# Kernel optimization log

Hardware: AMD Instinct MI355X
Metric: run time of the kernel (lower is better)

Reference implementation:

```python
import jax, jax.numpy as jnp
import numpy as np

N_NODES = 50000
N_REL = 500
D_IN = 128
D_OUT = 128
D_REL = 128
NHEADS = 2
ALPHA = 0.2
E1 = 200000   # direct edges
E2 = 50000    # 2-hop paths


def _xavier(key, shape, gain=1.414):
    fan_out, fan_in = shape[-2], shape[-1]
    a = gain * np.sqrt(6.0 / (fan_in + fan_out))
    return jax.random.uniform(key, shape, jnp.float32, -a, a)


def setup_inputs() -> dict:
    key = jax.random.key(0)
    ks = jax.random.split(key, 11)
    return {
        "entity_embeddings": jax.random.normal(ks[0], (N_NODES, D_IN), jnp.float32),
        "relation_embeddings": jax.random.normal(ks[1], (N_REL, D_REL), jnp.float32),
        "entity_list": jax.random.randint(ks[2], (2, E1), 0, N_NODES),
        "relation_type": jax.random.randint(ks[3], (E1,), 0, N_REL),
        "entity_list_nhop": jax.random.randint(ks[4], (2, E2), 0, N_NODES),
        "relation_type_nhop": jax.random.randint(ks[5], (E2, 2), 0, N_REL),
        # per-head attention params: a [out, 2*in + nrela], a2 [out] (squeezed [1,out])
        "a_heads": _xavier(ks[6], (NHEADS, D_OUT, 2 * D_IN + D_REL)),
        "a2_heads": _xavier(ks[7], (NHEADS, 1, D_OUT))[:, 0, :],
        "W": _xavier(ks[8], (D_REL, NHEADS * D_OUT)),
        "a_out": _xavier(ks[9], (NHEADS * D_OUT, 3 * NHEADS * D_OUT)),
        "a2_out": _xavier(ks[10], (1, NHEADS * D_OUT))[0],
    }


def _sp_att(x, edge, eemb, a, a2, concat):
    """SpGraphAttentionLayer. x:[N,Din] edge:[2,E] eemb:[E,Drel] a:[Dout,2Din+Drel] a2:[Dout]."""
    din = x.shape[1]
    src = x[edge[0]]                       # [E, Din]
    dst = x[edge[1]]                       # [E, Din]
    # a.mm(edge_h) without materializing the [E, 2Din+Drel] concat
    edge_m = (src @ a[:, :din].T
              + dst @ a[:, din:2 * din].T
              + eemb @ a[:, 2 * din:].T)   # [E, Dout]
    edge_e = jnp.exp(-jax.nn.leaky_relu(edge_m @ a2, ALPHA))      # [E]
    rowsum = jax.ops.segment_sum(edge_e, edge[0], num_segments=x.shape[0])  # [N]
    rowsum = jnp.where(rowsum == 0.0, 1e-12, rowsum)
    h = jax.ops.segment_sum(edge_e[:, None] * edge_m, edge[0], num_segments=x.shape[0])
    h = h / rowsum[:, None]                # [N, Dout]
    return jax.nn.elu(h) if concat else h


def reference(entity_embeddings, relation_embeddings, entity_list, relation_type,
              entity_list_nhop, relation_type_nhop, a_heads, a2_heads, W, a_out, a2_out):
    ent, rel = entity_embeddings, relation_embeddings
    edge_all = jnp.concatenate([entity_list, entity_list_nhop], axis=1)   # [2, E1+E2]

    # layer-1 edge embeddings
    emb_nhop = (rel[relation_type_nhop[:, 0]] + rel[relation_type_nhop[:, 1]]
                + ent[entity_list_nhop[0]] + ent[entity_list_nhop[1]])
    edge_embed = rel[relation_type] + ent[entity_list[0]] + ent[entity_list[1]]
    eemb1 = jnp.concatenate([edge_embed, emb_nhop], axis=0)               # [E1+E2, Drel]

    # multi-head sparse attention, concat heads (torch.cat dim=1 == (N,H,D)->reshape)
    heads = jax.vmap(lambda a, a2: _sp_att(ent, edge_all, eemb1, a, a2, True))(a_heads, a2_heads)
    out1 = jnp.transpose(heads, (1, 0, 2)).reshape(ent.shape[0], -1)      # [N, H*Dout]
    # dropout p=0.0 -> identity

    out_rel = rel @ W                                                      # [R, H*Dout]
    edge_embed2 = out_rel[relation_type]
    emb_nhop2 = (out_rel[relation_type_nhop[:, 0]] + out_rel[relation_type_nhop[:, 1]]
                 + out1[entity_list_nhop[0]] + out1[entity_list_nhop[1]])
    eemb2 = jnp.concatenate([edge_embed2, emb_nhop2], axis=0)

    out_ent = jax.nn.elu(_sp_att(out1, edge_all, eemb2, a_out, a2_out, False))
    return out_ent, out_rel
```

## Files before the change

kernel.cpp:

```cpp
#include <hip/hip_runtime.h>
#include <math.h>

#define NN   50000
#define NR   500
#define E1N  200000
#define E2N  50000
#define EN   250000
#define ALPHAC 0.2f

#define OFF_OUT1  ((size_t)0)
#define OFF_EE1   ((size_t)51200000)
#define OFF_EE2   ((size_t)53200000)
#define OFF_W1    ((size_t)54200000)
#define OFF_W2    ((size_t)54203072)
#define OFF_DEG   ((size_t)54206144)
#define OFF_OFFS  ((size_t)54406144)
#define OFF_CUR   ((size_t)54606208)
#define OFF_BSUM  ((size_t)54806208)
#define OFF_CARRY ((size_t)54807232)
#define OFF_CSR   ((size_t)54808256)
#define OFF_AHH   ((size_t)55808256)
#define OFF_AHL   ((size_t)56004864)
#define OFF_AOH   ((size_t)56201472)
#define OFF_AOL   ((size_t)56594688)

typedef __attribute__((ext_vector_type(8))) short bf16x8;
typedef __attribute__((ext_vector_type(4))) short short4v;
typedef __attribute__((ext_vector_type(2))) short short2v;
typedef __attribute__((ext_vector_type(4))) float f4;
typedef __attribute__((ext_vector_type(2))) float f2;
typedef __attribute__((ext_vector_type(4))) float f32x4;

__device__ __forceinline__ float lrelu(float x) { return x > 0.f ? x : ALPHAC * x; }
__device__ __forceinline__ float eluf(float x)  { return x > 0.f ? x : expm1f(x); }

__device__ __forceinline__ short bfh(float x) {
    union { float f; unsigned u; } c; c.f = x;
    unsigned r = (c.u + 0x7FFFu + ((c.u >> 16) & 1u)) >> 16;
    return (short)r;
}
__device__ __forceinline__ float bf2f(short h) {
    union { unsigned u; float f; } c; c.u = ((unsigned)(unsigned short)h) << 16;
    return c.f;
}

__device__ __forceinline__ void decode_edge(int e, const int* el1, const int* rt1,
                                            const int* el2, const int* rtn,
                                            int& src, int& dst, int& ra, int& rb) {
    if (e < E1N) {
        src = el1[e]; dst = el1[E1N + e]; ra = rt1[e]; rb = -1;
    } else {
        int j = e - E1N;
        src = el2[j]; dst = el2[E2N + j]; ra = rtn[2 * j]; rb = rtn[2 * j + 1];
    }
}

__global__ void k_w(const float* aH, const float* a2H, const float* aO, const float* a2O,
                    float* w1, float* w2) {
    int t = blockIdx.x * blockDim.x + threadIdx.x;
    if (t < 768) {
        int h = t / 384; int r = t - h * 384; int seg = r >> 7; int j = r & 127;
        const float* A  = aH + (size_t)h * 128 * 384;
        const float* a2 = a2H + h * 128;
        float s = 0.f;
        for (int d = 0; d < 128; ++d) {
            const float* row = A + d * 384;
            float c;
            if (seg == 0)      c = row[j]       + row[256 + j];
            else if (seg == 1) c = row[128 + j] + row[256 + j];
            else               c = row[256 + j];
            s += a2[d] * c;
        }
        w1[t] = s;
    } else if (t < 1536) {
        int r = t - 768; int seg = r >> 8; int j = r & 255;
        float s = 0.f;
        for (int d = 0; d < 256; ++d) s += a2O[d] * aO[d * 768 + seg * 256 + j];
        w2[r] = s;
    }
}

__global__ void k_conv(const float* aH, const float* aO,
                       short* ahh, short* ahl, short* aoh, short* aol) {
    int t = blockIdx.x * 256 + threadIdx.x;
    if (t < 98304) {
        float x = aH[t];
        short hi = bfh(x);
        ahh[t] = hi; ahl[t] = bfh(x - bf2f(hi));
    } else if (t < 294912) {
        int i = t - 98304;
        float x = aO[i];
        short hi = bfh(x);
        aoh[i] = hi; aol[i] = bfh(x - bf2f(hi));
    }
}

__global__ void k_outrel(const float* rel, const float* W, float* outrel) {
    int r = blockIdx.x; int c = threadIdx.x;
    const float* rr = rel + r * 128;
    float s = 0.f;
    for (int k = 0; k < 128; ++k) s += rr[k] * W[k * 256 + c];
    outrel[r * 256 + c] = s;
}

__global__ void k_deg(const int* el1, const int* el2, int* deg) {
    int e = blockIdx.x * 256 + threadIdx.x;
    if (e >= EN) return;
    int src = (e < E1N) ? el1[e] : el2[e - E1N];
    atomicAdd(&deg[src], 1);
}

__global__ void k_scan1(const int* deg, int* offs, int* bsum) {
    __shared__ int s[256];
    int t = threadIdx.x; int i = blockIdx.x * 256 + t;
    int v = (i < NN) ? deg[i] : 0;
    s[t] = v; __syncthreads();
    for (int off = 1; off < 256; off <<= 1) {
        int x = (t >= off) ? s[t - off] : 0;
        __syncthreads(); s[t] += x; __syncthreads();
    }
    if (i < NN) offs[i] = s[t] - v;
    if (t == 255) bsum[blockIdx.x] = s[255];
}

__global__ void k_scan2(int* bsum, int* carry) {
    __shared__ int s[256];
    int t = threadIdx.x;
    int v = (t < 196) ? bsum[t] : 0;
    s[t] = v; __syncthreads();
    for (int off = 1; off < 256; off <<= 1) {
        int x = (t >= off) ? s[t - off] : 0;
        __syncthreads(); s[t] += x; __syncthreads();
    }
    if (t < 196) carry[t] = s[t] - v;
}

__global__ void k_scan3(int* offs, const int* carry) {
    int i = blockIdx.x * 256 + threadIdx.x;
    if (i < NN) offs[i] += carry[blockIdx.x];
}

__global__ void k_scatter(const int* el1, const int* el2, const int* offs,
                          int* cursor, int* csr) {
    int e = blockIdx.x * 256 + threadIdx.x;
    if (e >= EN) return;
    int src = (e < E1N) ? el1[e] : el2[e - E1N];
    int pos = offs[src] + atomicAdd(&cursor[src], 1);
    csr[pos] = e;
}

__global__ void k_ee1(const float* ent, const float* rel,
                      const int* el1, const int* rt1, const int* el2, const int* rtn,
                      const float* w1, float* ee) {
    int wid  = (blockIdx.x * blockDim.x + threadIdx.x) >> 6;
    int lane = threadIdx.x & 63;
    int e0 = wid * 8;
    if (e0 >= EN) return;
    f2 wA0 = *(const f2*)&w1[2 * lane];
    f2 wB0 = *(const f2*)&w1[128 + 2 * lane];
    f2 wC0 = *(const f2*)&w1[256 + 2 * lane];
    f2 wA1 = *(const f2*)&w1[384 + 2 * lane];
    f2 wB1 = *(const f2*)&w1[512 + 2 * lane];
    f2 wC1 = *(const f2*)&w1[640 + 2 * lane];
    int eend = min(e0 + 8, EN);
    for (int e = e0; e < eend; ++e) {
        int src, dst, ra, rb;
        decode_edge(e, el1, rt1, el2, rtn, src, dst, ra, rb);
        f2 es = *(const f2*)&ent[src * 128 + 2 * lane];
        f2 ed = *(const f2*)&ent[dst * 128 + 2 * lane];
        f2 rp = *(const f2*)&rel[ra * 128 + 2 * lane];
        if (rb >= 0) rp += *(const f2*)&rel[rb * 128 + 2 * lane];
        float t0 = es[0] * wA0[0] + es[1] * wA0[1] + ed[0] * wB0[0] + ed[1] * wB0[1]
                 + rp[0] * wC0[0] + rp[1] * wC0[1];
        float t1 = es[0] * wA1[0] + es[1] * wA1[1] + ed[0] * wB1[0] + ed[1] * wB1[1]
                 + rp[0] * wC1[0] + rp[1] * wC1[1];
        #pragma unroll
        for (int off = 32; off; off >>= 1) {
            t0 += __shfl_xor(t0, off, 64);
            t1 += __shfl_xor(t1, off, 64);
        }
        if (lane == 0) {
            ee[e]      = expf(-lrelu(t0));
            ee[EN + e] = expf(-lrelu(t1));
        }
    }
}

#define PK1 392
__global__ __launch_bounds__(512) void k_agg1(
        const float* ent, const float* rel,
        const int* el1, const int* rt1, const int* el2, const int* rtn,
        const int* offs, const int* csr, const float* ee,
        const short* ahh, const short* ahl, float* out1) {
    __shared__ __align__(16) short Yh[16 * 2 * PK1];
    __shared__ __align__(16) short Yl[16 * 2 * PK1];
    __shared__ float RS[16][2];
    int w = threadIdx.x >> 6;
    int lane = threadIdx.x & 63;
    for (int s = 0; s < 2; ++s) {
        int m = w * 2 + s;
        int n = blockIdx.x * 16 + m;
        int start = offs[n];
        int end = (n == NN - 1) ? EN : offs[n + 1];
        f2 en = *(const f2*)&ent[n * 128 + 2 * lane];
        f2 s2a = {0, 0}, sea = {0, 0}, s2b = {0, 0}, seb = {0, 0};
        float rs0 = 0.f, rs1 = 0.f;
        for (int idx = start; idx < end; ++idx) {
            int e = csr[idx];
            int src, dst, ra, rb;
            decode_edge(e, el1, rt1, el2, rtn, src, dst, ra, rb);
            float e0v = ee[e], e1v = ee[EN + e];
            f2 gg = *(const f2*)&ent[dst * 128 + 2 * lane];
            f2 rp = *(const f2*)&rel[ra * 128 + 2 * lane];
            if (rb >= 0) rp += *(const f2*)&rel[rb * 128 + 2 * lane];
            f2 em = rp + en + gg;
            s2a += e0v * gg; sea += e0v * em;
            s2b += e1v * gg; seb += e1v * em;
            rs0 += e0v; rs1 += e1v;
        }
        f2 regs[2][3] = {{rs0 * en, s2a, sea}, {rs1 * en, s2b, seb}};
        #pragma unroll
        for (int hh = 0; hh < 2; ++hh) {
            #pragma unroll
            for (int rg = 0; rg < 3; ++rg) {
                int base = m * 2 * PK1 + hh * PK1 + rg * 128 + 2 * lane;
                short2v vh, vl;
                #pragma unroll
                for (int j = 0; j < 2; ++j) {
                    float v = regs[hh][rg][j];
                    vh[j] = bfh(v);
                    vl[j] = bfh(v - bf2f(vh[j]));
                }
                *(short2v*)&Yh[base] = vh;
                *(short2v*)&Yl[base] = vl;
            }
        }
        if (lane == 0) { RS[m][0] = rs0; RS[m][1] = rs1; }
    }
    __syncthreads();

    int r = lane & 15, g = lane >> 4;
    int h = w >> 2;
    const short* YhB = &Yh[r * 2 * PK1 + h * PK1];
    const short* YlB = &Yl[r * 2 * PK1 + h * PK1];
    int ct0 = 2 * w, ct1 = 2 * w + 1;
    const short* B0h = ahh + (size_t)(ct0 * 16 + r) * 384;
    const short* B0l = ahl + (size_t)(ct0 * 16 + r) * 384;
    const short* B1h = ahh + (size_t)(ct1 * 16 + r) * 384;
    const short* B1l = ahl + (size_t)(ct1 * 16 + r) * 384;
    f32x4 z = {0.f, 0.f, 0.f, 0.f};
    f32x4 hh0 = z, hl0 = z, lh0 = z, hh1 = z, hl1 = z, lh1 = z;
    for (int kt = 0; kt < 12; ++kt) {
        int ko = kt * 32 + g * 8;
        bf16x8 yh = *(const bf16x8*)(YhB + ko);
        bf16x8 yl = *(const bf16x8*)(YlB + ko);
        bf16x8 b0h = *(const bf16x8*)(B0h + ko);
        bf16x8 b0l = *(const bf16x8*)(B0l + ko);
        bf16x8 b1h = *(const bf16x8*)(B1h + ko);
        bf16x8 b1l = *(const bf16x8*)(B1l + ko);
        hh0 = __builtin_amdgcn_mfma_f32_16x16x32_bf16(yh, b0h, hh0, 0, 0, 0);
        hh1 = __builtin_amdgcn_mfma_f32_16x16x32_bf16(yh, b1h, hh1, 0, 0, 0);
        hl0 = __builtin_amdgcn_mfma_f32_16x16x32_bf16(yl, b0h, hl0, 0, 0, 0);
        hl1 = __builtin_amdgcn_mfma_f32_16x16x32_bf16(yl, b1h, hl1, 0, 0, 0);
        lh0 = __builtin_amdgcn_mfma_f32_16x16x32_bf16(yh, b0l, lh0, 0, 0, 0);
        lh1 = __builtin_amdgcn_mfma_f32_16x16x32_bf16(yh, b1l, lh1, 0, 0, 0);
    }
    f32x4 acc0 = hh0 + hl0 + lh0;
    f32x4 acc1 = hh1 + hl1 + lh1;
    #pragma unroll
    for (int q = 0; q < 4; ++q) {
        int m = g * 4 + q;
        float rs = RS[m][h];
        float denom = (rs == 0.f) ? 1e-12f : rs;
        size_t row = (size_t)(blockIdx.x * 16 + m) * 256;
        out1[row + ct0 * 16 + r] = eluf(acc0[q] / denom);
        out1[row + ct1 * 16 + r] = eluf(acc1[q] / denom);
    }
}

__global__ void k_ee2(const float* out1, const float* orel,
                      const int* el1, const int* rt1, const int* el2, const int* rtn,
                      const float* w2, float* ee2) {
    int wid  = (blockIdx.x * blockDim.x + threadIdx.x) >> 6;
    int lane = threadIdx.x & 63;
    int e0 = wid * 8;
    if (e0 >= EN) return;
    f4 wS = *(const f4*)&w2[4 * lane];
    f4 wD = *(const f4*)&w2[256 + 4 * lane];
    f4 wE = *(const f4*)&w2[512 + 4 * lane];
    int eend = min(e0 + 8, EN);
    for (int e = e0; e < eend; ++e) {
        int src, dst, ra, rb;
        decode_edge(e, el1, rt1, el2, rtn, src, dst, ra, rb);
        f4 xs = *(const f4*)&out1[(size_t)src * 256 + 4 * lane];
        f4 xd = *(const f4*)&out1[(size_t)dst * 256 + 4 * lane];
        f4 em = *(const f4*)&orel[ra * 256 + 4 * lane];
        if (rb >= 0) em += *(const f4*)&orel[rb * 256 + 4 * lane] + xs + xd;
        f4 tv = xs * wS + xd * wD + em * wE;
        float t = tv[0] + tv[1] + tv[2] + tv[3];
        #pragma unroll
        for (int off = 32; off; off >>= 1) t += __shfl_xor(t, off, 64);
        if (lane == 0) ee2[e] = expf(-lrelu(t));
    }
}

#define PK2 776
__global__ __launch_bounds__(512) void k_agg2(
        const float* out1, const float* orel,
        const int* el1, const int* rt1, const int* el2, const int* rtn,
        const int* offs, const int* csr, const float* ee2,
        const short* aoh, const short* aol, float* out_ent) {
    __shared__ __align__(16) short Yh[16 * PK2];
    __shared__ __align__(16) short Yl[16 * PK2];
    __shared__ float RS[16];
    int w = threadIdx.x >> 6;
    int lane = threadIdx.x & 63;
    for (int s = 0; s < 2; ++s) {
        int m = w * 2 + s;
        int n = blockIdx.x * 16 + m;
        int start = offs[n];
        int end = (n == NN - 1) ? EN : offs[n + 1];
        f4 on = *(const f4*)&out1[(size_t)n * 256 + 4 * lane];
        f4 s2 = {0, 0, 0, 0}, se = {0, 0, 0, 0};
        float rs = 0.f;
        for (int idx = start; idx < end; ++idx) {
            int e = csr[idx];
            int src, dst, ra, rb;
            decode_edge(e, el1, rt1, el2, rtn, src, dst, ra, rb);
            float ev = ee2[e];
            f4 gg = *(const f4*)&out1[(size_t)dst * 256 + 4 * lane];
            f4 em = *(const f4*)&orel[ra * 256 + 4 * lane];
            if (rb >= 0) em += *(const f4*)&orel[rb * 256 + 4 * lane] + on + gg;
            s2 += ev * gg;
            se += ev * em;
            rs += ev;
        }
        f4 regs[3] = {rs * on, s2, se};
        #pragma unroll
        for (int rg = 0; rg < 3; ++rg) {
            int base = m * PK2 + rg * 256 + 4 * lane;
            short4v vh, vl;
            #pragma unroll
            for (int j = 0; j < 4; ++j) {
                float v = regs[rg][j];
                vh[j] = bfh(v);
                vl[j] = bfh(v - bf2f(vh[j]));
            }
            *(short4v*)&Yh[base] = vh;
            *(short4v*)&Yl[base] = vl;
        }
        if (lane == 0) RS[m] = rs;
    }
    __syncthreads();

    int r = lane & 15, g = lane >> 4;
    const short* YhB = &Yh[r * PK2];
    const short* YlB = &Yl[r * PK2];
    int ct0 = 2 * w, ct1 = 2 * w + 1;
    const short* B0h = aoh + (size_t)(ct0 * 16 + r) * 768;
    const short* B0l = aol + (size_t)(ct0 * 16 + r) * 768;
    const short* B1h = aoh + (size_t)(ct1 * 16 + r) * 768;
    const short* B1l = aol + (size_t)(ct1 * 16 + r) * 768;
    f32x4 z = {0.f, 0.f, 0.f, 0.f};
    f32x4 hh0 = z, hl0 = z, lh0 = z, hh1 = z, hl1 = z, lh1 = z;
    for (int kt = 0; kt < 24; ++kt) {
        int ko = kt * 32 + g * 8;
        bf16x8 yh = *(const bf16x8*)(YhB + ko);
        bf16x8 yl = *(const bf16x8*)(YlB + ko);
        bf16x8 b0h = *(const bf16x8*)(B0h + ko);
        bf16x8 b0l = *(const bf16x8*)(B0l + ko);
        bf16x8 b1h = *(const bf16x8*)(B1h + ko);
        bf16x8 b1l = *(const bf16x8*)(B1l + ko);
        hh0 = __builtin_amdgcn_mfma_f32_16x16x32_bf16(yh, b0h, hh0, 0, 0, 0);
        hh1 = __builtin_amdgcn_mfma_f32_16x16x32_bf16(yh, b1h, hh1, 0, 0, 0);
        hl0 = __builtin_amdgcn_mfma_f32_16x16x32_bf16(yl, b0h, hl0, 0, 0, 0);
        hl1 = __builtin_amdgcn_mfma_f32_16x16x32_bf16(yl, b1h, hl1, 0, 0, 0);
        lh0 = __builtin_amdgcn_mfma_f32_16x16x32_bf16(yh, b0l, lh0, 0, 0, 0);
        lh1 = __builtin_amdgcn_mfma_f32_16x16x32_bf16(yh, b1l, lh1, 0, 0, 0);
    }
    f32x4 acc0 = hh0 + hl0 + lh0;
    f32x4 acc1 = hh1 + hl1 + lh1;
    #pragma unroll
    for (int q = 0; q < 4; ++q) {
        int m = g * 4 + q;
        float rs = RS[m];
        float denom = (rs == 0.f) ? 1e-12f : rs;
        size_t row = (size_t)(blockIdx.x * 16 + m) * 256;
        out_ent[row + ct0 * 16 + r] = eluf(acc0[q] / denom);
        out_ent[row + ct1 * 16 + r] = eluf(acc1[q] / denom);
    }
}

extern "C" void kernel_launch(void* const* d_in, const int* in_sizes, int n_in,
                              void* d_out, int out_size, void* d_ws, size_t ws_size,
                              hipStream_t stream) {
    const float* ent = (const float*)d_in[0];
    const float* rel = (const float*)d_in[1];
    const int*   el1 = (const int*)d_in[2];
    const int*   rt1 = (const int*)d_in[3];
    const int*   el2 = (const int*)d_in[4];
    const int*   rtn = (const int*)d_in[5];
    const float* aH  = (const float*)d_in[6];
    const float* a2H = (const float*)d_in[7];
    const float* W   = (const float*)d_in[8];
    const float* aO  = (const float*)d_in[9];
    const float* a2O = (const float*)d_in[10];

    float* out_ent = (float*)d_out;
    float* out_rel = (float*)d_out + (size_t)NN * 256;

    char* ws = (char*)d_ws;
    float* out1   = (float*)(ws + OFF_OUT1);
    float* ee1b   = (float*)(ws + OFF_EE1);
    float* ee2b   = (float*)(ws + OFF_EE2);
    float* w1     = (float*)(ws + OFF_W1);
    float* w2     = (float*)(ws + OFF_W2);
    int*   deg    = (int*)(ws + OFF_DEG);
    int*   offs   = (int*)(ws + OFF_OFFS);
    int*   cur    = (int*)(ws + OFF_CUR);
    int*   bsum   = (int*)(ws + OFF_BSUM);
    int*   carry  = (int*)(ws + OFF_CARRY);
    int*   csr    = (int*)(ws + OFF_CSR);
    short* ahh    = (short*)(ws + OFF_AHH);
    short* ahl    = (short*)(ws + OFF_AHL);
    short* aoh    = (short*)(ws + OFF_AOH);
    short* aol    = (short*)(ws + OFF_AOL);

    hipMemsetAsync(deg, 0, (size_t)NN * 4, stream);
    hipMemsetAsync(cur, 0, (size_t)NN * 4, stream);

    k_w<<<6, 256, 0, stream>>>(aH, a2H, aO, a2O, w1, w2);
    k_conv<<<1152, 256, 0, stream>>>(aH, aO, ahh, ahl, aoh, aol);
    k_outrel<<<NR, 256, 0, stream>>>(rel, W, out_rel);

    k_deg<<<(EN + 255) / 256, 256, 0, stream>>>(el1, el2, deg);
    k_scan1<<<(NN + 255) / 256, 256, 0, stream>>>(deg, offs, bsum);
    k_scan2<<<1, 256, 0, stream>>>(bsum, carry);
    k_scan3<<<(NN + 255) / 256, 256, 0, stream>>>(offs, carry);
    k_scatter<<<(EN + 255) / 256, 256, 0, stream>>>(el1, el2, offs, cur, csr);

    int ee_blocks = (EN / 8 + 3) / 4 + 1;
    k_ee1<<<ee_blocks, 256, 0, stream>>>(ent, rel, el1, rt1, el2, rtn, w1, ee1b);
    k_agg1<<<NN / 16, 512, 0, stream>>>(ent, rel, el1, rt1, el2, rtn,
                                        offs, csr, ee1b, ahh, ahl, out1);
    k_ee2<<<ee_blocks, 256, 0, stream>>>(out1, out_rel, el1, rt1, el2, rtn, w2, ee2b);
    k_agg2<<<NN / 16, 512, 0, stream>>>(out1, out_rel, el1, rt1, el2, rtn,
                                        offs, csr, ee2b, aoh, aol, out_ent);
}
```

Before: 780.4 us.

## Double aggregation block size to one wave per node and tile

The two aggregation kernels now launch 1024 threads per block instead of 512. Each of the 16 waves gathers one destination node rather than two, then computes one 16-column MFMA output tile instead of two. This raises the number of waves available to hide the irregular gather latency and halves the per-wave accumulator registers. The cost is fewer co-resident blocks per CU and larger barrier groups. Separately, the layer-1 edge-score kernel switches from float2 loads at 2*lane to two scalar loads at lane and lane+64, giving fully coalesced 256-byte row accesses.

Result: faster. 753.9 us (-3.4%).

```diff
diff --git a/kernel.cpp b/kernel.cpp
--- a/kernel.cpp
+++ b/kernel.cpp
@@ -156,24 +156,23 @@
     int lane = threadIdx.x & 63;
     int e0 = wid * 8;
     if (e0 >= EN) return;
-    f2 wA0 = *(const f2*)&w1[2 * lane];
-    f2 wB0 = *(const f2*)&w1[128 + 2 * lane];
-    f2 wC0 = *(const f2*)&w1[256 + 2 * lane];
-    f2 wA1 = *(const f2*)&w1[384 + 2 * lane];
-    f2 wB1 = *(const f2*)&w1[512 + 2 * lane];
-    f2 wC1 = *(const f2*)&w1[640 + 2 * lane];
+    int d0 = lane, d1 = lane + 64;
+    float wA00 = w1[d0],       wA01 = w1[d1];
+    float wB00 = w1[128 + d0], wB01 = w1[128 + d1];
+    float wC00 = w1[256 + d0], wC01 = w1[256 + d1];
+    float wA10 = w1[384 + d0], wA11 = w1[384 + d1];
+    float wB10 = w1[512 + d0], wB11 = w1[512 + d1];
+    float wC10 = w1[640 + d0], wC11 = w1[640 + d1];
     int eend = min(e0 + 8, EN);
     for (int e = e0; e < eend; ++e) {
         int src, dst, ra, rb;
         decode_edge(e, el1, rt1, el2, rtn, src, dst, ra, rb);
-        f2 es = *(const f2*)&ent[src * 128 + 2 * lane];
-        f2 ed = *(const f2*)&ent[dst * 128 + 2 * lane];
-        f2 rp = *(const f2*)&rel[ra * 128 + 2 * lane];
-        if (rb >= 0) rp += *(const f2*)&rel[rb * 128 + 2 * lane];
-        float t0 = es[0] * wA0[0] + es[1] * wA0[1] + ed[0] * wB0[0] + ed[1] * wB0[1]
-                 + rp[0] * wC0[0] + rp[1] * wC0[1];
-        float t1 = es[0] * wA1[0] + es[1] * wA1[1] + ed[0] * wB1[0] + ed[1] * wB1[1]
-                 + rp[0] * wC1[0] + rp[1] * wC1[1];
+        float es0 = ent[src * 128 + d0], es1 = ent[src * 128 + d1];
+        float ed0 = ent[dst * 128 + d0], ed1 = ent[dst * 128 + d1];
+        float rp0 = rel[ra * 128 + d0],  rp1 = rel[ra * 128 + d1];
+        if (rb >= 0) { rp0 += rel[rb * 128 + d0]; rp1 += rel[rb * 128 + d1]; }
+        float t0 = es0 * wA00 + es1 * wA01 + ed0 * wB00 + ed1 * wB01 + rp0 * wC00 + rp1 * wC01;
+        float t1 = es0 * wA10 + es1 * wA11 + ed0 * wB10 + ed1 * wB11 + rp0 * wC10 + rp1 * wC11;
         #pragma unroll
         for (int off = 32; off; off >>= 1) {
             t0 += __shfl_xor(t0, off, 64);
@@ -187,7 +186,7 @@
 }
 
 #define PK1 392
-__global__ __launch_bounds__(512) void k_agg1(
+__global__ __launch_bounds__(1024) void k_agg1(
         const float* ent, const float* rel,
         const int* el1, const int* rt1, const int* el2, const int* rtn,
         const int* offs, const int* csr, const float* ee,
@@ -197,8 +196,8 @@
     __shared__ float RS[16][2];
     int w = threadIdx.x >> 6;
     int lane = threadIdx.x & 63;
-    for (int s = 0; s < 2; ++s) {
-        int m = w * 2 + s;
+    {
+        int m = w;
         int n = blockIdx.x * 16 + m;
         int start = offs[n];
         int end = (n == NN - 1) ? EN : offs[n + 1];
@@ -240,41 +239,32 @@
     __syncthreads();
 
     int r = lane & 15, g = lane >> 4;
-    int h = w >> 2;
+    int ct = w;
+    int h = w >> 3;
     const short* YhB = &Yh[r * 2 * PK1 + h * PK1];
     const short* YlB = &Yl[r * 2 * PK1 + h * PK1];
-    int ct0 = 2 * w, ct1 = 2 * w + 1;
-    const short* B0h = ahh + (size_t)(ct0 * 16 + r) * 384;
-    const short* B0l = ahl + (size_t)(ct0 * 16 + r) * 384;
-    const short* B1h = ahh + (size_t)(ct1 * 16 + r) * 384;
-    const short* B1l = ahl + (size_t)(ct1 * 16 + r) * 384;
+    const short* B0h = ahh + (size_t)(ct * 16 + r) * 384;
+    const short* B0l = ahl + (size_t)(ct * 16 + r) * 384;
     f32x4 z = {0.f, 0.f, 0.f, 0.f};
-    f32x4 hh0 = z, hl0 = z, lh0 = z, hh1 = z, hl1 = z, lh1 = z;
+    f32x4 hh0 = z, hl0 = z, lh0 = z;
     for (int kt = 0; kt < 12; ++kt) {
         int ko = kt * 32 + g * 8;
         bf16x8 yh = *(const bf16x8*)(YhB + ko);
         bf16x8 yl = *(const bf16x8*)(YlB + ko);
         bf16x8 b0h = *(const bf16x8*)(B0h + ko);
         bf16x8 b0l = *(const bf16x8*)(B0l + ko);
-        bf16x8 b1h = *(const bf16x8*)(B1h + ko);
-        bf16x8 b1l = *(const bf16x8*)(B1l + ko);
         hh0 = __builtin_amdgcn_mfma_f32_16x16x32_bf16(yh, b0h, hh0, 0, 0, 0);
-        hh1 = __builtin_amdgcn_mfma_f32_16x16x32_bf16(yh, b1h, hh1, 0, 0, 0);
         hl0 = __builtin_amdgcn_mfma_f32_16x16x32_bf16(yl, b0h, hl0, 0, 0, 0);
-        hl1 = __builtin_amdgcn_mfma_f32_16x16x32_bf16(yl, b1h, hl1, 0, 0, 0);
         lh0 = __builtin_amdgcn_mfma_f32_16x16x32_bf16(yh, b0l, lh0, 0, 0, 0);
-        lh1 = __builtin_amdgcn_mfma_f32_16x16x32_bf16(yh, b1l, lh1, 0, 0, 0);
     }
     f32x4 acc0 = hh0 + hl0 + lh0;
-    f32x4 acc1 = hh1 + hl1 + lh1;
     #pragma unroll
     for (int q = 0; q < 4; ++q) {
         int m = g * 4 + q;
         float rs = RS[m][h];
         float denom = (rs == 0.f) ? 1e-12f : rs;
         size_t row = (size_t)(blockIdx.x * 16 + m) * 256;
-        out1[row + ct0 * 16 + r] = eluf(acc0[q] / denom);
-        out1[row + ct1 * 16 + r] = eluf(acc1[q] / denom);
+        out1[row + ct * 16 + r] = eluf(acc0[q] / denom);
     }
 }
 
@@ -305,7 +295,7 @@
 }
 
 #define PK2 776
-__global__ __launch_bounds__(512) void k_agg2(
+__global__ __launch_bounds__(1024) void k_agg2(
         const float* out1, const float* orel,
         const int* el1, const int* rt1, const int* el2, const int* rtn,
         const int* offs, const int* csr, const float* ee2,
@@ -315,8 +305,8 @@
     __shared__ float RS[16];
     int w = threadIdx.x >> 6;
     int lane = threadIdx.x & 63;
-    for (int s = 0; s < 2; ++s) {
-        int m = w * 2 + s;
+    {
+        int m = w;
         int n = blockIdx.x * 16 + m;
         int start = offs[n];
         int end = (n == NN - 1) ? EN : offs[n + 1];
@@ -354,40 +344,31 @@
     __syncthreads();
 
     int r = lane & 15, g = lane >> 4;
+    int ct = w;
     const short* YhB = &Yh[r * PK2];
     const short* YlB = &Yl[r * PK2];
-    int ct0 = 2 * w, ct1 = 2 * w + 1;
-    const short* B0h = aoh + (size_t)(ct0 * 16 + r) * 768;
-    const short* B0l = aol + (size_t)(ct0 * 16 + r) * 768;
-    const short* B1h = aoh + (size_t)(ct1 * 16 + r) * 768;
-    const short* B1l = aol + (size_t)(ct1 * 16 + r) * 768;
+    const short* B0h = aoh + (size_t)(ct * 16 + r) * 768;
+    const short* B0l = aol + (size_t)(ct * 16 + r) * 768;
     f32x4 z = {0.f, 0.f, 0.f, 0.f};
-    f32x4 hh0 = z, hl0 = z, lh0 = z, hh1 = z, hl1 = z, lh1 = z;
+    f32x4 hh0 = z, hl0 = z, lh0 = z;
     for (int kt = 0; kt < 24; ++kt) {
         int ko = kt * 32 + g * 8;
         bf16x8 yh = *(const bf16x8*)(YhB + ko);
         bf16x8 yl = *(const bf16x8*)(YlB + ko);
         bf16x8 b0h = *(const bf16x8*)(B0h + ko);
         bf16x8 b0l = *(const bf16x8*)(B0l + ko);
-        bf16x8 b1h = *(const bf16x8*)(B1h + ko);
-        bf16x8 b1l = *(const bf16x8*)(B1l + ko);
         hh0 = __builtin_amdgcn_mfma_f32_16x16x32_bf16(yh, b0h, hh0, 0, 0, 0);
-        hh1 = __builtin_amdgcn_mfma_f32_16x16x32_bf16(yh, b1h, hh1, 0, 0, 0);
         hl0 = __builtin_amdgcn_mfma_f32_16x16x32_bf16(yl, b0h, hl0, 0, 0, 0);
-        hl1 = __builtin_amdgcn_mfma_f32_16x16x32_bf16(yl, b1h, hl1, 0, 0, 0);
         lh0 = __builtin_amdgcn_mfma_f32_16x16x32_bf16(yh, b0l, lh0, 0, 0, 0);
-        lh1 = __builtin_amdgcn_mfma_f32_16x16x32_bf16(yh, b1l, lh1, 0, 0, 0);
     }
     f32x4 acc0 = hh0 + hl0 + lh0;
-    f32x4 acc1 = hh1 + hl1 + lh1;
     #pragma unroll
     for (int q = 0; q < 4; ++q) {
         int m = g * 4 + q;
         float rs = RS[m];
         float denom = (rs == 0.f) ? 1e-12f : rs;
         size_t row = (size_t)(blockIdx.x * 16 + m) * 256;
-        out_ent[row + ct0 * 16 + r] = eluf(acc0[q] / denom);
-        out_ent[row + ct1 * 16 + r] = eluf(acc1[q] / denom);
+        out_ent[row + ct * 16 + r] = eluf(acc0[q] / denom);
     }
 }
 
@@ -441,9 +422,9 @@
 
     int ee_blocks = (EN / 8 + 3) / 4 + 1;
     k_ee1<<<ee_blocks, 256, 0, stream>>>(ent, rel, el1, rt1, el2, rtn, w1, ee1b);
-    k_agg1<<<NN / 16, 512, 0, stream>>>(ent, rel, el1, rt1, el2, rtn,
-                                        offs, csr, ee1b, ahh, ahl, out1);
+    k_agg1<<<NN / 16, 1024, 0, stream>>>(ent, rel, el1, rt1, el2, rtn,
+                                         offs, csr, ee1b, ahh, ahl, out1);
     k_ee2<<<ee_blocks, 256, 0, stream>>>(out1, out_rel, el1, rt1, el2, rtn, w2, ee2b);
-    k_agg2<<<NN / 16, 512, 0, stream>>>(out1, out_rel, el1, rt1, el2, rtn,
-                                        offs, csr, ee2b, aoh, aol, out_ent);
-}
+    k_agg2<<<NN / 16, 1024, 0, stream>>>(out1, out_rel, el1, rt1, el2, rtn,
+                                         offs, csr, ee2b, aoh, aol, out_ent);
+}
```
